# Kernel tuning notes

Hardware: AMD Instinct MI355X
Metric: run time of the kernel (lower is better)

## Reference

```python
import jax, jax.numpy as jnp
import numpy as np

# SO(2)-equivariant linear (eSCN, arXiv:2302.03655), 'uv' fully-connected mode.
# Irreps l = 0..4 on both input and output sides.
LS = (0, 1, 2, 3, 4)
N, C_IN, C_OUT = 8192, 128, 128


def _build_paths():
    """Enumerate sparse-product entries (in_idx, out_idx, weight_idx, coef).

    Per (l_in, l_out) path: one weight for m=0, and for each 1<=m<=min(l_in,l_out)
    a (w_re, w_im) pair acting as the 2x2 rotation
        y_{+m} = w_re x_{+m} - w_im x_{-m}
        y_{-m} = w_im x_{+m} + w_re x_{-m}
    path_norm scales every path into an output irrep by 1/sqrt(#paths).
    """
    dims = [2 * l + 1 for l in LS]
    off = np.concatenate([[0], np.cumsum(dims)[:-1]])  # start of each irrep block
    pn = 1.0 / np.sqrt(len(LS))  # every output irrep receives len(LS) paths
    in_idx, out_idx, w_idx, coef = [], [], [], []
    w = 0
    for lo_i, lo in enumerate(LS):
        for li_i, li in enumerate(LS):
            oi, oo = int(off[li_i]), int(off[lo_i])
            # m = 0 component (index l within a (2l+1) block)
            in_idx.append(oi + li); out_idx.append(oo + lo); w_idx.append(w); coef.append(pn)
            w += 1
            for m in range(1, min(li, lo) + 1):
                ip, im = oi + li + m, oi + li - m   # input +m / -m positions
                op, om = oo + lo + m, oo + lo - m   # output +m / -m positions
                w_re, w_im = w, w + 1
                w += 2
                for ii, jj, ww, s in ((ip, op, w_re, 1.0), (im, om, w_re, 1.0),
                                      (ip, om, w_im, 1.0), (im, op, w_im, -1.0)):
                    in_idx.append(ii); out_idx.append(jj); w_idx.append(ww); coef.append(s * pn)
    return (np.asarray(in_idx), np.asarray(out_idx), np.asarray(w_idx),
            np.asarray(coef, np.float32), w, int(sum(dims)))


IN_IDX, OUT_IDX, W_IDX, COEF, NUM_W, DIM = _build_paths()  # NUM_W=85, DIM=25, T=145


def setup_inputs() -> dict:
    key = jax.random.key(0)
    k1, k2 = jax.random.split(key)
    x = jax.random.normal(k1, (N, DIM, C_IN), jnp.float32)
    wgt = jax.random.normal(k2, (NUM_W, C_IN, C_OUT), jnp.float32) * (C_IN ** -0.5)
    return {"input": x, "weight": wgt}


def reference(input, weight):
    coef = jnp.asarray(COEF)
    # gather one row per sparse-product entry: [N, T, C_in]
    x = input[:, IN_IDX, :] * coef[None, :, None]
    # per-entry vec-mat with the entry's weight matrix: [N, T, C_out]
    y = jnp.einsum('ntc,tcd->ntd', x, weight[W_IDX])
    # scatter-add entries into their output irrep components
    out = jnp.zeros((input.shape[0], DIM, weight.shape[-1]), y.dtype)
    return out.at[:, OUT_IDX, :].add(y)
```

## Files before the change

### kernel.cpp

```cpp
#include <hip/hip_runtime.h>
#include <cstdint>
#include <cstddef>

#define NROWS 8192
#define DIM   25
#define CIN   128
#define COUT  128
#define MAXT  160

struct Tables {
  int   w_idx[MAXT];
  float coef[MAXT];
  int   o_start[DIM + 1];
  int   e_in[MAXT];
  int   e_t[MAXT];
  int   T;
};

constexpr Tables build_tables() {
  Tables tb{};
  int off[5] = {0, 1, 4, 9, 16};
  const float pn = 0.44721359549995793f;
  int in_idx[MAXT] = {}, out_idx[MAXT] = {}, widx[MAXT] = {};
  float cf[MAXT] = {};
  int T = 0, w = 0;
  for (int lo = 0; lo < 5; ++lo) {
    for (int li = 0; li < 5; ++li) {
      int oi = off[li], oo = off[lo];
      in_idx[T] = oi + li; out_idx[T] = oo + lo; widx[T] = w; cf[T] = pn; ++T; ++w;
      int mm = li < lo ? li : lo;
      for (int m = 1; m <= mm; ++m) {
        int ip = oi + li + m, im = oi + li - m;
        int op = oo + lo + m, om = oo + lo - m;
        int wre = w, wim = w + 1; w += 2;
        in_idx[T] = ip; out_idx[T] = op; widx[T] = wre; cf[T] = pn;  ++T;
        in_idx[T] = im; out_idx[T] = om; widx[T] = wre; cf[T] = pn;  ++T;
        in_idx[T] = ip; out_idx[T] = om; widx[T] = wim; cf[T] = pn;  ++T;
        in_idx[T] = im; out_idx[T] = op; widx[T] = wim; cf[T] = -pn; ++T;
      }
    }
  }
  tb.T = T;
  for (int t = 0; t < T; ++t) { tb.w_idx[t] = widx[t]; tb.coef[t] = cf[t]; }
  int pos = 0;
  for (int o = 0; o < DIM; ++o) {
    tb.o_start[o] = pos;
    for (int t = 0; t < T; ++t)
      if (out_idx[t] == o) { tb.e_in[pos] = in_idx[t]; tb.e_t[pos] = t; ++pos; }
  }
  tb.o_start[DIM] = pos;
  return tb;
}

__constant__ Tables TAB = build_tables();

__device__ __forceinline__ uint16_t f2bf(float f) {
  uint32_t u = __float_as_uint(f);
  uint32_t r = (u + 0x7FFFu + ((u >> 16) & 1u)) >> 16;
  return (uint16_t)r;
}

__device__ __forceinline__ void load_lds16(const void* g, void* l) {
  __builtin_amdgcn_global_load_lds(
      (const __attribute__((address_space(1))) uint32_t*)g,
      (__attribute__((address_space(3))) uint32_t*)l, 16, 0, 0);
}

typedef __bf16 v8bf __attribute__((ext_vector_type(8)));
typedef float  v4f  __attribute__((ext_vector_type(4)));

#define NCVT (NROWS * DIM * CIN / 4 / 512)
#define NWB  (145 * 4)

__global__ void prep_kernel(const float* __restrict__ X, uint16_t* __restrict__ Y,
                            const float* __restrict__ W, uint16_t* __restrict__ Bt) {
  if (blockIdx.x < NCVT) {
    int i0 = blockIdx.x * 512 + threadIdx.x;
    #pragma unroll
    for (int r = 0; r < 2; ++r) {
      int i = i0 + (r << 8);
      float4 v = ((const float4*)X)[i];
      ushort4 o;
      o.x = f2bf(v.x); o.y = f2bf(v.y); o.z = f2bf(v.z); o.w = f2bf(v.w);
      ((ushort4*)Y)[i] = o;
    }
  } else {
    __shared__ float tile[128][33];
    int b  = blockIdx.x - NCVT;
    int t  = b >> 2;
    int d0 = (b & 3) << 5;
    int w  = TAB.w_idx[t];
    float cf = TAB.coef[t];
    const float* Wp = W + (size_t)w * CIN * COUT;
    uint16_t* Bp = Bt + (size_t)t * CIN * COUT;
    int tid = threadIdx.x;
    {
      int dcol = tid & 31, cbase = tid >> 5;
      #pragma unroll
      for (int r = 0; r < 16; ++r) {
        int c = (r << 3) + cbase;
        tile[c][dcol] = cf * Wp[(size_t)c * COUT + d0 + dcol];
      }
    }
    __syncthreads();
    {
      int c = tid & 127, dbase = tid >> 7;
      #pragma unroll
      for (int r = 0; r < 16; ++r) {
        int dd = (r << 1) + dbase;
        Bp[(size_t)(d0 + dd) * CIN + c] = f2bf(tile[c][dd]);
      }
    }
  }
}

__global__ __launch_bounds__(512) void so2_gemm(
    const uint16_t* __restrict__ Xb,
    const uint16_t* __restrict__ Bt,
    float* __restrict__ Out) {
  __shared__ __align__(16) uint16_t As[256 * 64];
  __shared__ __align__(16) uint16_t Bs[128 * 64];

  const int lb   = blockIdx.x;
  const int xcd  = lb & 7;
  const int slot = lb >> 3;
  const int o    = slot % 25;
  const int nt   = xcd + ((slot / 25) << 3);
  const int n0   = nt << 8;

  const int e0 = TAB.o_start[o];
  const int nE = TAB.o_start[o + 1] - e0;

  const int tid  = threadIdx.x;
  const int w    = tid >> 6;
  const int l    = tid & 63;

  const int srow = (w << 3) + (l >> 3);
  const int slt  = l & 7;
  const int ssrc = ((slt ^ (l >> 3)) << 3);

  const int lr   = l & 15;
  const int quad = l >> 4;
  const int wr   = (w & 3) << 6;
  const int wc   = (w >> 2) << 6;

  v4f acc[4][4];
  #pragma unroll
  for (int i = 0; i < 4; ++i)
    #pragma unroll
    for (int j = 0; j < 4; ++j)
      acc[i][j] = v4f{0.f, 0.f, 0.f, 0.f};

  const int nIter = nE << 1;
  for (int ki = 0; ki < nIter; ++ki) {
    const int e    = e0 + (ki >> 1);
    const int kk   = (ki & 1) << 6;
    const int irow = TAB.e_in[e];
    const int trow = TAB.e_t[e];

    const uint16_t* gA = Xb + ((size_t)(n0 + srow) * DIM + irow) * CIN + kk + ssrc;
    const uint16_t* gB = Bt + ((size_t)trow * COUT + srow) * CIN + kk + ssrc;

    if (ki) __syncthreads();
    #pragma unroll
    for (int j = 0; j < 4; ++j) {
      const int m = (j << 6) + srow;
      load_lds16(gA + (size_t)(j << 6) * (DIM * CIN), &As[m * 64 + slt * 8]);
    }
    #pragma unroll
    for (int j = 0; j < 2; ++j) {
      const int m = (j << 6) + srow;
      load_lds16(gB + (size_t)(j << 6) * CIN, &Bs[m * 64 + slt * 8]);
    }
    __syncthreads();

    #pragma unroll
    for (int kk2 = 0; kk2 < 2; ++kk2) {
      const int s = (((kk2 << 2) + quad) ^ (lr & 7)) << 3;
      v8bf a[4], b[4];
      #pragma unroll
      for (int i = 0; i < 4; ++i) {
        a[i] = *(const v8bf*)(&As[(wr + (i << 4) + lr) * 64 + s]);
        b[i] = *(const v8bf*)(&Bs[(wc + (i << 4) + lr) * 64 + s]);
      }
      #pragma unroll
      for (int i = 0; i < 4; ++i)
        #pragma unroll
        for (int j = 0; j < 4; ++j)
          acc[i][j] = __builtin_amdgcn_mfma_f32_16x16x32_bf16(a[i], b[j],
                                                              acc[i][j], 0, 0, 0);
    }
  }

  #pragma unroll
  for (int i = 0; i < 4; ++i) {
    #pragma unroll
    for (int r = 0; r < 4; ++r) {
      const int n = n0 + wr + (i << 4) + (quad << 2) + r;
      float* op = Out + ((size_t)n * DIM + o) * COUT + wc + lr;
      #pragma unroll
      for (int j = 0; j < 4; ++j)
        op[j << 4] = acc[i][j][r];
    }
  }
}

extern "C" void kernel_launch(void* const* d_in, const int* in_sizes, int n_in,
                              void* d_out, int out_size, void* d_ws, size_t ws_size,
                              hipStream_t stream) {
  const float* X = (const float*)d_in[0];
  const float* W = (const float*)d_in[1];
  float* Out = (float*)d_out;

  uint16_t* Xb = (uint16_t*)d_ws;
  uint16_t* Bt = (uint16_t*)((char*)d_ws + (size_t)NROWS * DIM * CIN * 2);

  prep_kernel<<<NCVT + NWB, 256, 0, stream>>>(X, Xb, W, Bt);
  so2_gemm<<<DIM * (NROWS / 256), 512, 0, stream>>>(Xb, Bt, Out);
}
```

Before: 235.9 us.

## Fuse X bf16 conversion into GEMM loads and double-buffer B tiles

Removes the separate pass that converts X to bf16 in workspace; the GEMM now loads fp32 X into registers, converts it, and writes bf16 into LDS, with next-iteration loads prefetched during MFMA. B tiles are double-buffered in LDS via direct global-to-LDS loads. This eliminates a full write and reread of the bf16 X copy but doubles the bytes of X gathered per GEMM iteration and adds register pressure and an extra barrier per step.

```diff
diff --git a/kernel.cpp b/kernel.cpp
--- a/kernel.cpp
+++ b/kernel.cpp
@@ -69,57 +69,50 @@
 typedef __bf16 v8bf __attribute__((ext_vector_type(8)));
 typedef float  v4f  __attribute__((ext_vector_type(4)));
 
-#define NCVT (NROWS * DIM * CIN / 4 / 512)
+__device__ __forceinline__ v8bf cvt8(float4 p, float4 q) {
+  v8bf v;
+  v[0] = (__bf16)p.x; v[1] = (__bf16)p.y; v[2] = (__bf16)p.z; v[3] = (__bf16)p.w;
+  v[4] = (__bf16)q.x; v[5] = (__bf16)q.y; v[6] = (__bf16)q.z; v[7] = (__bf16)q.w;
+  return v;
+}
+
 #define NWB  (145 * 4)
 
-__global__ void prep_kernel(const float* __restrict__ X, uint16_t* __restrict__ Y,
-                            const float* __restrict__ W, uint16_t* __restrict__ Bt) {
-  if (blockIdx.x < NCVT) {
-    int i0 = blockIdx.x * 512 + threadIdx.x;
-    #pragma unroll
-    for (int r = 0; r < 2; ++r) {
-      int i = i0 + (r << 8);
-      float4 v = ((const float4*)X)[i];
-      ushort4 o;
-      o.x = f2bf(v.x); o.y = f2bf(v.y); o.z = f2bf(v.z); o.w = f2bf(v.w);
-      ((ushort4*)Y)[i] = o;
-    }
-  } else {
-    __shared__ float tile[128][33];
-    int b  = blockIdx.x - NCVT;
-    int t  = b >> 2;
-    int d0 = (b & 3) << 5;
-    int w  = TAB.w_idx[t];
-    float cf = TAB.coef[t];
-    const float* Wp = W + (size_t)w * CIN * COUT;
-    uint16_t* Bp = Bt + (size_t)t * CIN * COUT;
-    int tid = threadIdx.x;
-    {
-      int dcol = tid & 31, cbase = tid >> 5;
-      #pragma unroll
-      for (int r = 0; r < 16; ++r) {
-        int c = (r << 3) + cbase;
-        tile[c][dcol] = cf * Wp[(size_t)c * COUT + d0 + dcol];
-      }
-    }
-    __syncthreads();
-    {
-      int c = tid & 127, dbase = tid >> 7;
-      #pragma unroll
-      for (int r = 0; r < 16; ++r) {
-        int dd = (r << 1) + dbase;
-        Bp[(size_t)(d0 + dd) * CIN + c] = f2bf(tile[c][dd]);
-      }
-    }
-  }
-}
-
-__global__ __launch_bounds__(512) void so2_gemm(
-    const uint16_t* __restrict__ Xb,
+__global__ void prep_kernel(const float* __restrict__ W, uint16_t* __restrict__ Bt) {
+  __shared__ float tile[128][33];
+  int b  = blockIdx.x;
+  int t  = b >> 2;
+  int d0 = (b & 3) << 5;
+  int w  = TAB.w_idx[t];
+  float cf = TAB.coef[t];
+  const float* Wp = W + (size_t)w * CIN * COUT;
+  uint16_t* Bp = Bt + (size_t)t * CIN * COUT;
+  int tid = threadIdx.x;
+  {
+    int dcol = tid & 31, cbase = tid >> 5;
+    #pragma unroll
+    for (int r = 0; r < 16; ++r) {
+      int c = (r << 3) + cbase;
+      tile[c][dcol] = cf * Wp[(size_t)c * COUT + d0 + dcol];
+    }
+  }
+  __syncthreads();
+  {
+    int c = tid & 127, dbase = tid >> 7;
+    #pragma unroll
+    for (int r = 0; r < 16; ++r) {
+      int dd = (r << 1) + dbase;
+      Bp[(size_t)(d0 + dd) * CIN + c] = f2bf(tile[c][dd]);
+    }
+  }
+}
+
+__global__ __launch_bounds__(512, 4) void so2_gemm(
+    const float* __restrict__ X,
     const uint16_t* __restrict__ Bt,
     float* __restrict__ Out) {
   __shared__ __align__(16) uint16_t As[256 * 64];
-  __shared__ __align__(16) uint16_t Bs[128 * 64];
+  __shared__ __align__(16) uint16_t Bs[2][128 * 64];
 
   const int lb   = blockIdx.x;
   const int xcd  = lb & 7;
@@ -139,6 +132,12 @@
   const int slt  = l & 7;
   const int ssrc = ((slt ^ (l >> 3)) << 3);
 
+  const int arow = tid >> 3;
+  const int achk = tid & 7;
+  const int aslt = achk ^ (arow & 7);
+  const float* gAbase = X + (size_t)(n0 + arow) * DIM * CIN + (achk << 3);
+  uint16_t* lAbase = &As[arow * 64 + aslt * 8];
+
   const int lr   = l & 15;
   const int quad = l >> 4;
   const int wr   = (w & 3) << 6;
@@ -152,27 +151,50 @@
       acc[i][j] = v4f{0.f, 0.f, 0.f, 0.f};
 
   const int nIter = nE << 1;
+
+  {
+    const int irow = TAB.e_in[e0];
+    const int trow = TAB.e_t[e0];
+    const uint16_t* gB = Bt + ((size_t)trow * COUT + srow) * CIN + ssrc;
+    load_lds16(gB,                    &Bs[0][srow * 64 + slt * 8]);
+    load_lds16(gB + (size_t)64 * CIN, &Bs[0][(64 + srow) * 64 + slt * 8]);
+
+    float4 a_st[8];
+    const float* gA = gAbase + (size_t)irow * CIN;
+    #pragma unroll
+    for (int j = 0; j < 4; ++j) {
+      const float4* p = (const float4*)(gA + (size_t)(j << 6) * (DIM * CIN));
+      a_st[2 * j]     = p[0];
+      a_st[2 * j + 1] = p[1];
+    }
+    #pragma unroll
+    for (int j = 0; j < 4; ++j)
+      *(v8bf*)(lAbase + (j << 6) * 64) = cvt8(a_st[2 * j], a_st[2 * j + 1]);
+  }
+  __syncthreads();
+
   for (int ki = 0; ki < nIter; ++ki) {
-    const int e    = e0 + (ki >> 1);
-    const int kk   = (ki & 1) << 6;
-    const int irow = TAB.e_in[e];
-    const int trow = TAB.e_t[e];
-
-    const uint16_t* gA = Xb + ((size_t)(n0 + srow) * DIM + irow) * CIN + kk + ssrc;
-    const uint16_t* gB = Bt + ((size_t)trow * COUT + srow) * CIN + kk + ssrc;
-
-    if (ki) __syncthreads();
-    #pragma unroll
-    for (int j = 0; j < 4; ++j) {
-      const int m = (j << 6) + srow;
-      load_lds16(gA + (size_t)(j << 6) * (DIM * CIN), &As[m * 64 + slt * 8]);
-    }
-    #pragma unroll
-    for (int j = 0; j < 2; ++j) {
-      const int m = (j << 6) + srow;
-      load_lds16(gB + (size_t)(j << 6) * CIN, &Bs[m * 64 + slt * 8]);
-    }
-    __syncthreads();
+    const int cur  = ki & 1;
+    const bool more = (ki + 1 < nIter);
+
+    float4 a_st[8];
+    if (more) {
+      const int kn   = ki + 1;
+      const int e    = e0 + (kn >> 1);
+      const int kk   = (kn & 1) << 6;
+      const int irow = TAB.e_in[e];
+      const int trow = TAB.e_t[e];
+      const uint16_t* gB = Bt + ((size_t)trow * COUT + srow) * CIN + kk + ssrc;
+      load_lds16(gB,                    &Bs[cur ^ 1][srow * 64 + slt * 8]);
+      load_lds16(gB + (size_t)64 * CIN, &Bs[cur ^ 1][(64 + srow) * 64 + slt * 8]);
+      const float* gA = gAbase + (size_t)irow * CIN + kk;
+      #pragma unroll
+      for (int j = 0; j < 4; ++j) {
+        const float4* p = (const float4*)(gA + (size_t)(j << 6) * (DIM * CIN));
+        a_st[2 * j]     = p[0];
+        a_st[2 * j + 1] = p[1];
+      }
+    }
 
     #pragma unroll
     for (int kk2 = 0; kk2 < 2; ++kk2) {
@@ -181,7 +203,7 @@
       #pragma unroll
       for (int i = 0; i < 4; ++i) {
         a[i] = *(const v8bf*)(&As[(wr + (i << 4) + lr) * 64 + s]);
-        b[i] = *(const v8bf*)(&Bs[(wc + (i << 4) + lr) * 64 + s]);
+        b[i] = *(const v8bf*)(&Bs[cur][(wc + (i << 4) + lr) * 64 + s]);
       }
       #pragma unroll
       for (int i = 0; i < 4; ++i)
@@ -189,6 +211,14 @@
         for (int j = 0; j < 4; ++j)
           acc[i][j] = __builtin_amdgcn_mfma_f32_16x16x32_bf16(a[i], b[j],
                                                               acc[i][j], 0, 0, 0);
+    }
+
+    if (more) {
+      __syncthreads();
+      #pragma unroll
+      for (int j = 0; j < 4; ++j)
+        *(v8bf*)(lAbase + (j << 6) * 64) = cvt8(a_st[2 * j], a_st[2 * j + 1]);
+      __syncthreads();
     }
   }
 
@@ -212,9 +242,8 @@
   const float* W = (const float*)d_in[1];
   float* Out = (float*)d_out;
 
-  uint16_t* Xb = (uint16_t*)d_ws;
-  uint16_t* Bt = (uint16_t*)((char*)d_ws + (size_t)NROWS * DIM * CIN * 2);
-
-  prep_kernel<<<NCVT + NWB, 256, 0, stream>>>(X, Xb, W, Bt);
-  so2_gemm<<<DIM * (NROWS / 256), 512, 0, stream>>>(Xb, Bt, Out);
-}
+  uint16_t* Bt = (uint16_t*)d_ws;
+
+  prep_kernel<<<NWB, 256, 0, stream>>>(W, Bt);
+  so2_gemm<<<DIM * (NROWS / 256), 512, 0, stream>>>(X, Bt, Out);
+}
```

Result: slower. 262.1 us (+11.1%).
